# Performance work log

Measured on AMD Instinct MI355X. Metric: run time of the kernel, lower is better.

The kernel has to match this reference:

```python
import jax, jax.numpy as jnp
import numpy as np
from jax import lax

T, D_IN, D_OUT = 8192, 4096, 4096
N_ADAPT, RANK = 8, 16


def setup_inputs() -> dict:
    key = jax.random.key(0)
    ks = jax.random.split(key, 6)
    x = jax.random.normal(ks[0], (T, D_IN), jnp.float32)
    weight_indices = jax.random.randint(ks[1], (T,), 0, N_ADAPT, jnp.int64 if jax.config.jax_enable_x64 else jnp.int32)
    W_base = jax.random.normal(ks[2], (D_OUT, D_IN), jnp.float32) * 0.02
    A_buffer = jax.random.normal(ks[3], (N_ADAPT, D_IN, RANK), jnp.float32) * 0.02
    B_buffer = jax.random.normal(ks[4], (N_ADAPT, RANK, D_OUT), jnp.float32) * 0.02
    DeltaW = jax.random.normal(ks[5], (N_ADAPT, D_IN, D_OUT), jnp.float32) * 0.02
    return {"x": x, "weight_indices": weight_indices, "W_base": W_base,
            "A_buffer": A_buffer, "B_buffer": B_buffer, "DeltaW": DeltaW}


def _ldmm(indices, x, A, B, D):
    """Per-token adapter matmul: out[t] = x[t] @ (DeltaW[j] + A[j] @ B[j]), j = indices[t].
    Grouped by adapter via masked GEMMs (fixed small adapter count), jit-friendly."""
    n_adapt = A.shape[0]
    acc0 = jnp.zeros((x.shape[0], D.shape[2]), x.dtype)

    def body(acc, inp):
        a_id, A_a, B_a, D_a = inp
        mask = (indices == a_id)[:, None]
        xm = jnp.where(mask, x, jnp.zeros((), x.dtype))  # [T, in]
        W_eff = D_a + A_a @ B_a                          # [in, out]
        return acc + xm @ W_eff, None

    acc, _ = lax.scan(body, acc0, (jnp.arange(n_adapt), A, B, D))
    return acc


def reference(x, weight_indices, W_base, A_buffer, B_buffer, DeltaW):
    base = x @ W_base.T                                   # ColumnParallelLinear
    delta = _ldmm(weight_indices, x, A_buffer, B_buffer, DeltaW)
    # NOTE: source has `base_output = +output` (unary plus, likely a typo for `+=`);
    # we implement the intended fused semantics base + ldmm.
    return base + delta
```

## Files before the change

### kernel.cpp

```cpp
#include <hip/hip_runtime.h>


#define T_TOKENS 8192
#define DIM 4096
#define NADAPT 8
#define RANK 16

#define BM2 256
#define MAXT2 40
#define GRIDX2 (MAXT2 * 16)

#define BM1 128
#define MAXT1 72

typedef __attribute__((ext_vector_type(8))) short bf16x8;
typedef __attribute__((ext_vector_type(4))) float f32x4;

__device__ __forceinline__ unsigned short f2bf(float f) {
  union { float f; unsigned u; } v; v.f = f;
  unsigned r = v.u + 0x7FFFu + ((v.u >> 16) & 1u);
  return (unsigned short)(r >> 16);
}

__device__ __forceinline__ void gload_lds16(const void* g, void* l) {
  __builtin_amdgcn_global_load_lds(
      (const __attribute__((address_space(1))) void*)g,
      (__attribute__((address_space(3))) void*)l, 16, 0, 0);
}

template <int N> __device__ __forceinline__ void vmwait() {
  if constexpr (N == 0)      asm volatile("s_waitcnt vmcnt(0)" ::: "memory");
  else if constexpr (N == 4) asm volatile("s_waitcnt vmcnt(4)" ::: "memory");
  else if constexpr (N == 8) asm volatile("s_waitcnt vmcnt(8)" ::: "memory");
}

__global__ void prep_kernel(const int* __restrict__ idx, int* __restrict__ perm,
                            int* __restrict__ meta, int padm) {
  __shared__ int s_cnt[NADAPT];
  __shared__ int s_padoff[NADAPT + 1];
  __shared__ int s_wsum[16];
  const int tid = threadIdx.x;
  const int lane = tid & 63;
  const int wave = tid >> 6;

  if (tid < NADAPT) s_cnt[tid] = 0;
  __syncthreads();
  for (int t = tid; t < T_TOKENS; t += 1024) atomicAdd(&s_cnt[idx[t]], 1);
  __syncthreads();

  if (tid == 0) {
    int off = 0, nt = 0;
    for (int j = 0; j < NADAPT; ++j) {
      meta[j] = s_cnt[j];
      s_padoff[j] = off;
      const int c = s_cnt[j];
      const int ntj = (c + padm - 1) / padm;
      for (int i = 0; i < ntj; ++i) {
        meta[32 + 3 * nt + 0] = j;
        meta[32 + 3 * nt + 1] = off + i * padm;
        meta[32 + 3 * nt + 2] = min(padm, c - i * padm);
        ++nt;
      }
      off += ntj * padm;
    }
    s_padoff[NADAPT] = off;
    meta[17] = nt;
    for (int j = 0; j <= NADAPT; ++j) meta[8 + j] = s_padoff[j];
  }
  __syncthreads();

  const int total_pad = s_padoff[NADAPT];
  for (int t = tid; t < total_pad; t += 1024) perm[t] = -1;
  __syncthreads();

  for (int j = 0; j < NADAPT; ++j) {
    int base = s_padoff[j];
    for (int c0 = 0; c0 < T_TOKENS; c0 += 1024) {
      const int t = c0 + tid;
      const int flag = (idx[t] == j) ? 1 : 0;
      const unsigned long long bal = __ballot(flag);
      const int wpos = __popcll(bal & ((1ULL << lane) - 1ULL));
      if (lane == 0) s_wsum[wave] = __popcll(bal);
      __syncthreads();
      int woff = 0, ctot = 0;
      for (int w = 0; w < 16; ++w) {
        const int v = s_wsum[w];
        if (w < wave) woff += v;
        ctot += v;
      }
      if (flag) perm[base + woff + wpos] = t;
      base += ctot;
      __syncthreads();
    }
  }
}

__global__ void convert_x_kernel(const float* __restrict__ x,
                                 unsigned short* __restrict__ xb) {
  const long long i = (long long)blockIdx.x * 256 + threadIdx.x;
  const float4* x4 = (const float4*)x;
  const float4 a = x4[2 * i];
  const float4 b = x4[2 * i + 1];
  uint4 o;
  o.x = (unsigned)f2bf(a.x) | ((unsigned)f2bf(a.y) << 16);
  o.y = (unsigned)f2bf(a.z) | ((unsigned)f2bf(a.w) << 16);
  o.z = (unsigned)f2bf(b.x) | ((unsigned)f2bf(b.y) << 16);
  o.w = (unsigned)f2bf(b.z) | ((unsigned)f2bf(b.w) << 16);
  ((uint4*)xb)[i] = o;
}

__global__ __launch_bounds__(256) void build_wtot_all_kernel(
    const float* __restrict__ Wb, const float* __restrict__ Am,
    const float* __restrict__ Bm, const float* __restrict__ DW,
    unsigned short* __restrict__ Wt) {
  const int i0 = blockIdx.x << 6;
  const int o0 = blockIdx.y << 6;
  __shared__ float Dl[2][64 * 64];
  __shared__ float Alt[2][16][68];
  __shared__ float Bl[2][16][68];
  const int tid = threadIdx.x;
  const int to = (tid >> 4) << 2;
  const int ti = (tid & 15) << 2;

  float4 wbr[4];
#pragma unroll
  for (int m = 0; m < 4; ++m)
    wbr[m] = *(const float4*)(Wb + (size_t)(o0 + to + m) * DIM + i0 + ti);

  const int di = tid >> 4;
  const int do4 = (tid & 15) << 2;
  const int ar_i = tid >> 2, ar_r4 = (tid & 3) << 2;
  const int br_r = tid >> 4, br_o4 = (tid & 15) << 2;

  float4 dwr[4], ar, brv;
  {
    const float* dwp = DW + (size_t)i0 * DIM + o0;
#pragma unroll
    for (int q = 0; q < 4; ++q)
      dwr[q] = *(const float4*)(dwp + (size_t)(q * 16 + di) * DIM + do4);
    ar = *(const float4*)(Am + ((size_t)(i0 + ar_i)) * RANK + ar_r4);
    brv = *(const float4*)(Bm + (size_t)br_r * DIM + o0 + br_o4);
  }
#pragma unroll
  for (int q = 0; q < 4; ++q) {
    const int i = q * 16 + di;
    const int iq = i >> 2, ie = i & 3;
#pragma unroll
    for (int k = 0; k < 4; ++k) {
      const int o = do4 + k;
      Dl[0][o * 64 + (((iq ^ (o & 15)) << 2) | ie)] = ((const float*)&dwr[q])[k];
    }
  }
#pragma unroll
  for (int k = 0; k < 4; ++k) Alt[0][ar_r4 + k][ar_i] = ((const float*)&ar)[k];
  *(float4*)&Bl[0][br_r][br_o4] = brv;
  __syncthreads();

  for (int j = 0; j < NADAPT; ++j) {
    const int pb = j & 1;
    if (j + 1 < NADAPT) {
      const float* dwp = DW + ((size_t)(j + 1) * DIM + i0) * DIM + o0;
#pragma unroll
      for (int q = 0; q < 4; ++q)
        dwr[q] = *(const float4*)(dwp + (size_t)(q * 16 + di) * DIM + do4);
      ar = *(const float4*)(Am + ((size_t)(j + 1) * DIM + i0 + ar_i) * RANK + ar_r4);
      brv = *(const float4*)(Bm + ((size_t)(j + 1) * RANK + br_r) * DIM + o0 + br_o4);
    }
    float acc[4][4];
#pragma unroll
    for (int m = 0; m < 4; ++m) {
      const int o = to + m;
      const float4 d = *(const float4*)&Dl[pb][o * 64 + (((ti >> 2) ^ (o & 15)) << 2)];
      acc[m][0] = wbr[m].x + d.x; acc[m][1] = wbr[m].y + d.y;
      acc[m][2] = wbr[m].z + d.z; acc[m][3] = wbr[m].w + d.w;
    }
#pragma unroll
    for (int r = 0; r < RANK; ++r) {
      const float4 av = *(const float4*)&Alt[pb][r][ti];
      const float4 bv = *(const float4*)&Bl[pb][r][to];
#pragma unroll
      for (int m = 0; m < 4; ++m) {
        const float b = ((const float*)&bv)[m];
        acc[m][0] += b * av.x; acc[m][1] += b * av.y;
        acc[m][2] += b * av.z; acc[m][3] += b * av.w;
      }
    }
#pragma unroll
    for (int m = 0; m < 4; ++m) {
      const int o = to + m;
      const unsigned lo = (unsigned)f2bf(acc[m][0]) | ((unsigned)f2bf(acc[m][1]) << 16);
      const unsigned hi = (unsigned)f2bf(acc[m][2]) | ((unsigned)f2bf(acc[m][3]) << 16);
      uint2 pk; pk.x = lo; pk.y = hi;
      *(uint2*)(Wt + ((size_t)j * DIM + o0 + o) * DIM + i0 + ti) = pk;
    }
    if (j + 1 < NADAPT) {
      const int nb = pb ^ 1;
#pragma unroll
      for (int q = 0; q < 4; ++q) {
        const int i = q * 16 + di;
        const int iq = i >> 2, ie = i & 3;
#pragma unroll
        for (int k = 0; k < 4; ++k) {
          const int o = do4 + k;
          Dl[nb][o * 64 + (((iq ^ (o & 15)) << 2) | ie)] = ((const float*)&dwr[q])[k];
        }
      }
#pragma unroll
      for (int k = 0; k < 4; ++k) Alt[nb][ar_r4 + k][ar_i] = ((const float*)&ar)[k];
      *(float4*)&Bl[nb][br_r][br_o4] = brv;
      __syncthreads();
    }
  }
}

__global__ __launch_bounds__(256) void build_wtot_kernel(
    const float* __restrict__ Wb, const float* __restrict__ Am,
    const float* __restrict__ Bm, const float* __restrict__ DW,
    unsigned short* __restrict__ Wt, int j0) {
  const int jj = blockIdx.z;
  const int j = j0 + jj;
  const int i0 = blockIdx.x << 6;
  const int o0 = blockIdx.y << 6;
  __shared__ float Dl[64 * 64];
  __shared__ float Alt[16][68];
  __shared__ float Bl[16][68];
  const int tid = threadIdx.x;

  const float* dwp = DW + ((size_t)j * DIM + i0) * DIM + o0;
#pragma unroll
  for (int q = 0; q < 4; ++q) {
    const int lin = q * 256 + tid;
    const int i = lin >> 4;
    const int o4 = (lin & 15) << 2;
    const float4 v = *(const float4*)(dwp + (size_t)i * DIM + o4);
    const int iq = i >> 2, ie = i & 3;
#pragma unroll
    for (int k = 0; k < 4; ++k) {
      const int o = o4 + k;
      Dl[o * 64 + (((iq ^ (o & 15)) << 2) | ie)] = ((const float*)&v)[k];
    }
  }
  {
    const int ai = tid >> 2, r4 = (tid & 3) << 2;
    const float4 v = *(const float4*)(Am + ((size_t)j * DIM + i0 + ai) * RANK + r4);
#pragma unroll
    for (int k = 0; k < 4; ++k) Alt[r4 + k][ai] = ((const float*)&v)[k];
  }
  {
    const int br = tid >> 4, bo4 = (tid & 15) << 2;
    const float4 v = *(const float4*)(Bm + ((size_t)j * RANK + br) * DIM + o0 + bo4);
    *(float4*)&Bl[br][bo4] = v;
  }
  __syncthreads();

  const int to = (tid >> 4) << 2;
  const int ti = (tid & 15) << 2;
  float acc[4][4];

#pragma unroll
  for (int m = 0; m < 4; ++m) {
    const int o = to + m;
    const float4 w = *(const float4*)(Wb + (size_t)(o0 + o) * DIM + i0 + ti);
    const float4 d = *(const float4*)&Dl[o * 64 + (((ti >> 2) ^ (o & 15)) << 2)];
    acc[m][0] = w.x + d.x; acc[m][1] = w.y + d.y;
    acc[m][2] = w.z + d.z; acc[m][3] = w.w + d.w;
  }
#pragma unroll
  for (int r = 0; r < RANK; ++r) {
    const float4 av = *(const float4*)&Alt[r][ti];
    const float4 bv = *(const float4*)&Bl[r][to];
#pragma unroll
    for (int m = 0; m < 4; ++m) {
      const float b = ((const float*)&bv)[m];
      acc[m][0] += b * av.x; acc[m][1] += b * av.y;
      acc[m][2] += b * av.z; acc[m][3] += b * av.w;
    }
  }
#pragma unroll
  for (int m = 0; m < 4; ++m) {
    const int o = to + m;
    const unsigned lo = (unsigned)f2bf(acc[m][0]) | ((unsigned)f2bf(acc[m][1]) << 16);
    const unsigned hi = (unsigned)f2bf(acc[m][2]) | ((unsigned)f2bf(acc[m][3]) << 16);
    uint2 pk; pk.x = lo; pk.y = hi;
    *(uint2*)(Wt + ((size_t)jj * DIM + o0 + o) * DIM + i0 + ti) = pk;
  }
}

template <int BUF, int KK, int MQ, int VME, int SGRP, int SOP, int SKH, bool DOST>
__device__ __forceinline__ void do_phase(
    char* smem, int tid, int stile,
    const unsigned short* const* aB, const unsigned short* const* bB,
    const int* aoff, const int* boff, bf16x8* bfr, f32x4 (*acc)[4]) {
  const int grp = (BUF * 2 + KK) * 16384;
  if constexpr (MQ == 0) {
#pragma unroll
    for (int n = 0; n < 4; ++n)
      bfr[n] = *(const bf16x8*)(smem + 65536 + grp + boff[n]);
  }
  bf16x8 afr[4];
#pragma unroll
  for (int i = 0; i < 4; ++i)
    afr[i] = *(const bf16x8*)(smem + grp + aoff[MQ * 4 + i]);
  if constexpr (DOST) {
    const unsigned short* const* bs = SOP ? bB : aB;
#pragma unroll
    for (int q = 0; q < 2; ++q)
      gload_lds16(bs[q] + stile * 64 + SKH * 32,
                  smem + SOP * 65536 + SGRP * 16384 + q * 8192 + tid * 16);
  }
  __builtin_amdgcn_s_barrier();
  asm volatile("s_waitcnt lgkmcnt(0)" ::: "memory");
  __builtin_amdgcn_s_setprio(1);
#pragma unroll
  for (int i = 0; i < 4; ++i)
#pragma unroll
    for (int n = 0; n < 4; ++n)
      acc[MQ * 4 + i][n] =
          __builtin_amdgcn_mfma_f32_16x16x32_bf16(afr[i], bfr[n], acc[MQ * 4 + i][n], 0, 0, 0);
  __builtin_amdgcn_s_setprio(0);
  vmwait<VME>();
  __builtin_amdgcn_s_barrier();
}

template <int SGRP, int SOP, int SKH>
__device__ __forceinline__ void do_stage(
    char* smem, int tid, int stile,
    const unsigned short* const* aB, const unsigned short* const* bB) {
  const unsigned short* const* bs = SOP ? bB : aB;
#pragma unroll
  for (int q = 0; q < 2; ++q)
    gload_lds16(bs[q] + stile * 64 + SKH * 32,
                smem + SOP * 65536 + SGRP * 16384 + q * 8192 + tid * 16);
}

__global__ __launch_bounds__(512, 2) void gemm8_kernel(
    const unsigned short* __restrict__ xb, const unsigned short* __restrict__ Wt,
    const int* __restrict__ perm, const int* __restrict__ meta,
    float* __restrict__ out, int j0, int npp) {
  extern __shared__ char smem[];
  const int ntiles = meta[17];
  const int flat = blockIdx.x;
  const int swz = (flat & 7) * (GRIDX2 / 8) + (flat >> 3);
  const int mt = swz >> 4;
  const int nt = swz & 15;
  if (mt >= ntiles) return;
  const int adapter = meta[32 + 3 * mt];
  if (adapter < j0 || adapter >= j0 + npp) return;
  const int slot = adapter - j0;
  const int pbase = meta[32 + 3 * mt + 1];
  const int nbase = nt << 8;

  const int tid = threadIdx.x;
  const int lane = tid & 63;
  const int wave = tid >> 6;
  const int wr = wave >> 2, wc = wave & 3;
  const int fr = lane & 15, kg = lane >> 4;

  int aoff[8], boff[4];
#pragma unroll
  for (int m = 0; m < 8; ++m) {
    const int row = wr * 128 + m * 16 + fr;
    const int r = row >> 1, hf = row & 1;
    const int c = ((hf << 2) | kg) ^ (r & 7);
    aoff[m] = r * 128 + c * 16;
  }
#pragma unroll
  for (int n = 0; n < 4; ++n) {
    const int row = wc * 64 + n * 16 + fr;
    const int r = row >> 1, hf = row & 1;
    const int c = ((hf << 2) | kg) ^ (r & 7);
    boff[n] = r * 128 + c * 16;
  }

  const unsigned short* aB[2];
  const unsigned short* bB[2];
#pragma unroll
  for (int q = 0; q < 2; ++q) {
    const int L = q * 512 + tid;
    const int r = L >> 3, c = L & 7;
    const int s = c ^ (r & 7);
    const int grow = 2 * r + (s >> 2);
    const int gk = (s & 3) << 3;
    int pr = perm[pbase + grow];
    if (pr < 0) pr = 0;
    aB[q] = xb + (size_t)pr * DIM + gk;
    bB[q] = Wt + ((size_t)slot * DIM + nbase + grow) * DIM + gk;
  }

  const f32x4 zero = {0.f, 0.f, 0.f, 0.f};
  f32x4 acc[8][4];
#pragma unroll
  for (int m = 0; m < 8; ++m)
#pragma unroll
    for (int n = 0; n < 4; ++n) acc[m][n] = zero;
  bf16x8 bfr[4];

  do_stage<0, 0, 0>(smem, tid, 0, aB, bB);
  do_stage<0, 1, 0>(smem, tid, 0, aB, bB);
  do_stage<1, 0, 1>(smem, tid, 0, aB, bB);
  do_stage<1, 1, 1>(smem, tid, 0, aB, bB);
  do_stage<2, 0, 0>(smem, tid, 1, aB, bB);
  do_stage<2, 1, 0>(smem, tid, 1, aB, bB);
  vmwait<8>();
  __builtin_amdgcn_s_barrier();

  for (int it = 0; it < 31; ++it) {
    const int t1 = 2 * it + 1, t2 = 2 * it + 2, t3 = 2 * it + 3;
    do_phase<0, 0, 0, -1, 3, 0, 1, true>(smem, tid, t1, aB, bB, aoff, boff, bfr, acc);
    do_phase<0, 0, 1,  8, 3, 1, 1, true>(smem, tid, t1, aB, bB, aoff, boff, bfr, acc);
    do_phase<0, 1, 0, -1, 0, 0, 0, true>(smem, tid, t2, aB, bB, aoff, boff, bfr, acc);
    do_phase<0, 1, 1,  8, 0, 1, 0, true>(smem, tid, t2, aB, bB, aoff, boff, bfr, acc);
    do_phase<1, 0, 0, -1, 1, 0, 1, true>(smem, tid, t2, aB, bB, aoff, boff, bfr, acc);
    do_phase<1, 0, 1,  8, 1, 1, 1, true>(smem, tid, t2, aB, bB, aoff, boff, bfr, acc);
    do_phase<1, 1, 0, -1, 2, 0, 0, true>(smem, tid, t3, aB, bB, aoff, boff, bfr, acc);
    do_phase<1, 1, 1,  8, 2, 1, 0, true>(smem, tid, t3, aB, bB, aoff, boff, bfr, acc);
  }
  do_phase<0, 0, 0, -1, 3, 0, 1, true >(smem, tid, 63, aB, bB, aoff, boff, bfr, acc);
  do_phase<0, 0, 1,  8, 3, 1, 1, true >(smem, tid, 63, aB, bB, aoff, boff, bfr, acc);
  do_phase<0, 1, 0, -1, 0, 0, 0, false>(smem, tid, 0,  aB, bB, aoff, boff, bfr, acc);
  do_phase<0, 1, 1,  4, 0, 0, 0, false>(smem, tid, 0,  aB, bB, aoff, boff, bfr, acc);
  do_phase<1, 0, 0, -1, 0, 0, 0, false>(smem, tid, 0,  aB, bB, aoff, boff, bfr, acc);
  do_phase<1, 0, 1,  0, 0, 0, 0, false>(smem, tid, 0,  aB, bB, aoff, boff, bfr, acc);
  do_phase<1, 1, 0, -1, 0, 0, 0, false>(smem, tid, 0,  aB, bB, aoff, boff, bfr, acc);
  do_phase<1, 1, 1, -1, 0, 0, 0, false>(smem, tid, 0,  aB, bB, aoff, boff, bfr, acc);

#pragma unroll
  for (int m = 0; m < 8; ++m) {
#pragma unroll
    for (int t = 0; t < 4; ++t) {
      const int rt = wr * 128 + m * 16 + kg * 4 + t;
      const int pr = perm[pbase + rt];
      if (pr < 0) continue;
      float* orow = out + (size_t)pr * DIM + nbase + wc * 64;
#pragma unroll
      for (int n = 0; n < 4; ++n) orow[n * 16 + fr] = acc[m][n][t];
    }
  }
}

template <bool USE_XB>
__global__ __launch_bounds__(256) void gemm_kernel(
    const unsigned short* __restrict__ xb, const float* __restrict__ xf,
    const unsigned short* __restrict__ Wt,
    const int* __restrict__ perm, const int* __restrict__ meta,
    float* __restrict__ out, int j0, int npp) {
  const int ntiles = meta[17];
  const int mt = blockIdx.x;
  if (mt >= ntiles) return;
  const int adapter = meta[32 + 3 * mt];
  if (adapter < j0 || adapter >= j0 + npp) return;
  const int slot = adapter - j0;
  const int nt = blockIdx.y;
  const int pbase = meta[32 + 3 * mt + 1];
  const int nbase = nt << 7;

  __shared__ __align__(16) unsigned short As[BM1 * 64];
  __shared__ __align__(16) unsigned short Bs[BM1 * 64];

  const int tid = threadIdx.x;
  const int lane = tid & 63;
  const int wave = tid >> 6;

  const unsigned short* aSrcB[4];
  const float* aSrcF[4];
  const unsigned short* bSrc[4];
  unsigned short* aDst[4];
  unsigned short* bDst[4];
#pragma unroll
  for (int q = 0; q < 4; ++q) {
    const int c = wave * 4 + q;
    const int r = c * 8 + (lane >> 3);
    int pr = perm[pbase + r];
    if (pr < 0) pr = 0;
    if (USE_XB) aSrcB[q] = xb + (size_t)pr * DIM + (lane & 7) * 8;
    else        aSrcF[q] = xf + (size_t)pr * DIM + (lane & 7) * 8;
    bSrc[q] = Wt + ((size_t)slot * DIM + nbase + r) * DIM + (lane & 7) * 8;
    aDst[q] = As + c * 512;
    bDst[q] = Bs + c * 512;
  }

  const int wr = wave >> 1, wc = wave & 1;
  const int fr = lane & 15, kg = lane >> 4;

  const f32x4 zero = {0.f, 0.f, 0.f, 0.f};
  f32x4 acc[4][4];
#pragma unroll
  for (int m = 0; m < 4; ++m)
#pragma unroll
    for (int n = 0; n < 4; ++n) acc[m][n] = zero;

  for (int k0 = 0; k0 < DIM; k0 += 64) {
    if (USE_XB) {
#pragma unroll
      for (int q = 0; q < 4; ++q) gload_lds16(aSrcB[q] + k0, aDst[q]);
    } else {
#pragma unroll
      for (int q = 0; q < 4; ++q) {
        const float4 va = *(const float4*)(aSrcF[q] + k0);
        const float4 vb = *(const float4*)(aSrcF[q] + k0 + 4);
        union { bf16x8 v; unsigned short s[8]; } u;
        u.s[0] = f2bf(va.x); u.s[1] = f2bf(va.y); u.s[2] = f2bf(va.z); u.s[3] = f2bf(va.w);
        u.s[4] = f2bf(vb.x); u.s[5] = f2bf(vb.y); u.s[6] = f2bf(vb.z); u.s[7] = f2bf(vb.w);
        *(bf16x8*)(aDst[q] + lane * 8) = u.v;
      }
    }
#pragma unroll
    for (int q = 0; q < 4; ++q) gload_lds16(bSrc[q] + k0, bDst[q]);
    __syncthreads();
#pragma unroll
    for (int kk = 0; kk < 2; ++kk) {
      bf16x8 a[4], b[4];
#pragma unroll
      for (int m = 0; m < 4; ++m)
        a[m] = *(const bf16x8*)(&As[(wr * 64 + m * 16 + fr) * 64 + kk * 32 + kg * 8]);
#pragma unroll
      for (int n = 0; n < 4; ++n)
        b[n] = *(const bf16x8*)(&Bs[(wc * 64 + n * 16 + fr) * 64 + kk * 32 + kg * 8]);
#pragma unroll
      for (int m = 0; m < 4; ++m)
#pragma unroll
        for (int n = 0; n < 4; ++n)
          acc[m][n] = __builtin_amdgcn_mfma_f32_16x16x32_bf16(a[m], b[n], acc[m][n], 0, 0, 0);
    }
    __syncthreads();
  }

#pragma unroll
  for (int m = 0; m < 4; ++m) {
#pragma unroll
    for (int t = 0; t < 4; ++t) {
      const int rt = wr * 64 + m * 16 + kg * 4 + t;
      const int pr = perm[pbase + rt];
      if (pr < 0) continue;
      float* orow = out + (size_t)pr * DIM + nbase + wc * 64;
#pragma unroll
      for (int n = 0; n < 4; ++n) orow[n * 16 + fr] = acc[m][n][t];
    }
  }
}

extern "C" void kernel_launch(void* const* d_in, const int* in_sizes, int n_in,
                              void* d_out, int out_size, void* d_ws, size_t ws_size,
                              hipStream_t stream) {
  const float* x  = (const float*)d_in[0];
  const int* widx = (const int*)d_in[1];
  const float* Wb = (const float*)d_in[2];
  const float* Am = (const float*)d_in[3];
  const float* Bm = (const float*)d_in[4];
  const float* DW = (const float*)d_in[5];
  float* out = (float*)d_out;

  const size_t XB_BYTES = (size_t)T_TOKENS * DIM * 2;
  const size_t WT1_BYTES = (size_t)DIM * DIM * 2;
  const size_t PM_BYTES = 16384 * sizeof(int) + 4096;

  int npp = 0;
  bool use_xb = true;
  for (int cand = NADAPT; cand >= 1; cand >>= 1) {
    if (XB_BYTES + (size_t)cand * WT1_BYTES + PM_BYTES <= ws_size) { npp = cand; break; }
  }
  if (npp == 0) { npp = 1; use_xb = false; }

  bool use8 = use_xb &&
      (hipFuncSetAttribute((const void*)gemm8_kernel,
                           hipFuncAttributeMaxDynamicSharedMemorySize, 131072) == hipSuccess);

  char* ws = (char*)d_ws;
  unsigned short* xb = (unsigned short*)ws;
  unsigned short* Wt = (unsigned short*)(ws + (use_xb ? XB_BYTES : 0));
  char* tail = (char*)Wt + (size_t)npp * WT1_BYTES;
  int* perm = (int*)tail;
  int* meta = (int*)(tail + 16384 * sizeof(int));

  prep_kernel<<<dim3(1), dim3(1024), 0, stream>>>(widx, perm, meta, use8 ? BM2 : BM1);
  if (use_xb)
    convert_x_kernel<<<dim3(T_TOKENS * DIM / (256 * 8)), dim3(256), 0, stream>>>(x, xb);

  if (npp == NADAPT) {
    build_wtot_all_kernel<<<dim3(DIM / 64, DIM / 64), dim3(256), 0, stream>>>(
        Wb, Am, Bm, DW, Wt);
    if (use8)
      gemm8_kernel<<<dim3(GRIDX2), dim3(512), 131072, stream>>>(
          xb, Wt, perm, meta, out, 0, NADAPT);
    else
      gemm_kernel<true><<<dim3(MAXT1, DIM / 128), dim3(256), 0, stream>>>(
          xb, nullptr, Wt, perm, meta, out, 0, NADAPT);
  } else {
    const int passes = NADAPT / npp;
    for (int p = 0; p < passes; ++p) {
      const int j0 = p * npp;
      build_wtot_kernel<<<dim3(DIM / 64, DIM / 64, npp), dim3(256), 0, stream>>>(
          Wb, Am, Bm, DW, Wt, j0);
      if (use_xb)
        gemm_kernel<true><<<dim3(MAXT1, DIM / 128), dim3(256), 0, stream>>>(
            xb, nullptr, Wt, perm, meta, out, j0, npp);
      else
        gemm_kernel<false><<<dim3(MAXT1, DIM / 128), dim3(256), 0, stream>>>(
            nullptr, x, Wt, perm, meta, out, j0, npp);
    }
  }
}
```

Measured before the change: 642.7 us.

## Split tail M-tiles into a separate 128-row kernel to balance the grid

```diff
diff --git a/kernel.cpp b/kernel.cpp
--- a/kernel.cpp
+++ b/kernel.cpp
@@ -8,7 +8,7 @@
 
 #define BM2 256
 #define MAXT2 40
-#define GRIDX2 (MAXT2 * 16)
+#define GRIDX2 512
 
 #define BM1 128
 #define MAXT1 72
@@ -438,6 +438,91 @@
   }
 }
 
+__global__ __launch_bounds__(256) void gemm_tail_kernel(
+    const unsigned short* __restrict__ xb, const unsigned short* __restrict__ Wt,
+    const int* __restrict__ perm, const int* __restrict__ meta,
+    float* __restrict__ out) {
+  const int ntiles = meta[17];
+  const int mt = 32 + (blockIdx.x >> 1);
+  if (mt >= ntiles) return;
+  const int half = blockIdx.x & 1;
+  const int adapter = meta[32 + 3 * mt];
+  const int pbase = meta[32 + 3 * mt + 1] + half * 128;
+  if (half * 128 >= meta[32 + 3 * mt + 2]) return;
+  const int nt = blockIdx.y;
+  const int nbase = nt << 7;
+
+  __shared__ __align__(16) unsigned short As[BM1 * 64];
+  __shared__ __align__(16) unsigned short Bs[BM1 * 64];
+
+  const int tid = threadIdx.x;
+  const int lane = tid & 63;
+  const int wave = tid >> 6;
+
+  const unsigned short* aSrcB[4];
+  const unsigned short* bSrc[4];
+  unsigned short* aDst[4];
+  unsigned short* bDst[4];
+#pragma unroll
+  for (int q = 0; q < 4; ++q) {
+    const int c = wave * 4 + q;
+    const int r = c * 8 + (lane >> 3);
+    int pr = perm[pbase + r];
+    if (pr < 0) pr = 0;
+    aSrcB[q] = xb + (size_t)pr * DIM + (lane & 7) * 8;
+    bSrc[q] = Wt + ((size_t)adapter * DIM + nbase + r) * DIM + (lane & 7) * 8;
+    aDst[q] = As + c * 512;
+    bDst[q] = Bs + c * 512;
+  }
+
+  const int wr = wave >> 1, wc = wave & 1;
+  const int fr = lane & 15, kg = lane >> 4;
+
+  const f32x4 zero = {0.f, 0.f, 0.f, 0.f};
+  f32x4 acc[4][4];
+#pragma unroll
+  for (int m = 0; m < 4; ++m)
+#pragma unroll
+    for (int n = 0; n < 4; ++n) acc[m][n] = zero;
+
+  for (int k0 = 0; k0 < DIM; k0 += 64) {
+#pragma unroll
+    for (int q = 0; q < 4; ++q) gload_lds16(aSrcB[q] + k0, aDst[q]);
+#pragma unroll
+    for (int q = 0; q < 4; ++q) gload_lds16(bSrc[q] + k0, bDst[q]);
+    __syncthreads();
+#pragma unroll
+    for (int kk = 0; kk < 2; ++kk) {
+      bf16x8 a[4], b[4];
+#pragma unroll
+      for (int m = 0; m < 4; ++m)
+        a[m] = *(const bf16x8*)(&As[(wr * 64 + m * 16 + fr) * 64 + kk * 32 + kg * 8]);
+#pragma unroll
+      for (int n = 0; n < 4; ++n)
+        b[n] = *(const bf16x8*)(&Bs[(wc * 64 + n * 16 + fr) * 64 + kk * 32 + kg * 8]);
+#pragma unroll
+      for (int m = 0; m < 4; ++m)
+#pragma unroll
+        for (int n = 0; n < 4; ++n)
+          acc[m][n] = __builtin_amdgcn_mfma_f32_16x16x32_bf16(a[m], b[n], acc[m][n], 0, 0, 0);
+    }
+    __syncthreads();
+  }
+
+#pragma unroll
+  for (int m = 0; m < 4; ++m) {
+#pragma unroll
+    for (int t = 0; t < 4; ++t) {
+      const int rt = wr * 64 + m * 16 + kg * 4 + t;
+      const int pr = perm[pbase + rt];
+      if (pr < 0) continue;
+      float* orow = out + (size_t)pr * DIM + nbase + wc * 64;
+#pragma unroll
+      for (int n = 0; n < 4; ++n) orow[n * 16 + fr] = acc[m][n][t];
+    }
+  }
+}
+
 template <bool USE_XB>
 __global__ __launch_bounds__(256) void gemm_kernel(
     const unsigned short* __restrict__ xb, const float* __restrict__ xf,
@@ -579,12 +664,15 @@
   if (npp == NADAPT) {
     build_wtot_all_kernel<<<dim3(DIM / 64, DIM / 64), dim3(256), 0, stream>>>(
         Wb, Am, Bm, DW, Wt);
-    if (use8)
+    if (use8) {
       gemm8_kernel<<<dim3(GRIDX2), dim3(512), 131072, stream>>>(
           xb, Wt, perm, meta, out, 0, NADAPT);
-    else
+      gemm_tail_kernel<<<dim3(16, DIM / 128), dim3(256), 0, stream>>>(
+          xb, Wt, perm, meta, out);
+    } else {
       gemm_kernel<true><<<dim3(MAXT1, DIM / 128), dim3(256), 0, stream>>>(
           xb, nullptr, Wt, perm, meta, out, 0, NADAPT);
+    }
   } else {
     const int passes = NADAPT / npp;
     for (int p = 0; p < passes; ++p) {
```

Result: no change. 632.8 us (-1.5%).

## Split tail M-tiles of grouped GEMM with split-K and atomic accumulation

Applied to the files above, without the earlier changes.

```diff
diff --git a/kernel.cpp b/kernel.cpp
--- a/kernel.cpp
+++ b/kernel.cpp
@@ -7,8 +7,7 @@
 #define RANK 16
 
 #define BM2 256
-#define MAXT2 40
-#define GRIDX2 (MAXT2 * 16)
+#define GRIDX2 512
 
 #define BM1 128
 #define MAXT1 72
@@ -95,6 +94,24 @@
   }
 }
 
+__global__ __launch_bounds__(256) void zero_tail_kernel(
+    const int* __restrict__ perm, const int* __restrict__ meta,
+    float* __restrict__ out) {
+  const int ntiles = meta[17];
+  const int mt = 32 + (int)(blockIdx.x >> 1);
+  if (mt >= ntiles) return;
+  const int half = blockIdx.x & 1;
+  const int pbase = meta[32 + 3 * mt + 1] + half * 128;
+  const int row = threadIdx.x >> 1;
+  const int c0 = blockIdx.y * 128 + (threadIdx.x & 1) * 64;
+  const int pr = perm[pbase + row];
+  if (pr < 0) return;
+  float4* p = (float4*)(out + (size_t)pr * DIM + c0);
+  const float4 z = {0.f, 0.f, 0.f, 0.f};
+#pragma unroll
+  for (int k = 0; k < 16; ++k) p[k] = z;
+}
+
 __global__ void convert_x_kernel(const float* __restrict__ x,
                                  unsigned short* __restrict__ xb) {
   const long long i = (long long)blockIdx.x * 256 + threadIdx.x;
@@ -333,22 +350,31 @@
                 smem + SOP * 65536 + SGRP * 16384 + q * 8192 + tid * 16);
 }
 
+template <int NTILES, bool TAILK>
 __global__ __launch_bounds__(512, 2) void gemm8_kernel(
     const unsigned short* __restrict__ xb, const unsigned short* __restrict__ Wt,
     const int* __restrict__ perm, const int* __restrict__ meta,
-    float* __restrict__ out, int j0, int npp) {
+    float* __restrict__ out) {
   extern __shared__ char smem[];
   const int ntiles = meta[17];
   const int flat = blockIdx.x;
-  const int swz = (flat & 7) * (GRIDX2 / 8) + (flat >> 3);
-  const int mt = swz >> 4;
-  const int nt = swz & 15;
+  int mt, nt, kc;
+  if (TAILK) {
+    kc = flat >> 7;
+    const int r = flat & 127;
+    mt = 32 + (r >> 4);
+    nt = r & 15;
+  } else {
+    const int swz = (flat & 7) * (GRIDX2 / 8) + (flat >> 3);
+    mt = swz >> 4;
+    nt = swz & 15;
+    kc = 0;
+  }
   if (mt >= ntiles) return;
   const int adapter = meta[32 + 3 * mt];
-  if (adapter < j0 || adapter >= j0 + npp) return;
-  const int slot = adapter - j0;
   const int pbase = meta[32 + 3 * mt + 1];
   const int nbase = nt << 8;
+  const size_t kbase = (size_t)kc * (NTILES * 64);
 
   const int tid = threadIdx.x;
   const int lane = tid & 63;
@@ -383,8 +409,8 @@
     const int gk = (s & 3) << 3;
     int pr = perm[pbase + grow];
     if (pr < 0) pr = 0;
-    aB[q] = xb + (size_t)pr * DIM + gk;
-    bB[q] = Wt + ((size_t)slot * DIM + nbase + grow) * DIM + gk;
+    aB[q] = xb + (size_t)pr * DIM + gk + kbase;
+    bB[q] = Wt + ((size_t)adapter * DIM + nbase + grow) * DIM + gk + kbase;
   }
 
   const f32x4 zero = {0.f, 0.f, 0.f, 0.f};
@@ -404,7 +430,7 @@
   vmwait<8>();
   __builtin_amdgcn_s_barrier();
 
-  for (int it = 0; it < 31; ++it) {
+  for (int it = 0; it < NTILES / 2 - 1; ++it) {
     const int t1 = 2 * it + 1, t2 = 2 * it + 2, t3 = 2 * it + 3;
     do_phase<0, 0, 0, -1, 3, 0, 1, true>(smem, tid, t1, aB, bB, aoff, boff, bfr, acc);
     do_phase<0, 0, 1,  8, 3, 1, 1, true>(smem, tid, t1, aB, bB, aoff, boff, bfr, acc);
@@ -415,14 +441,14 @@
     do_phase<1, 1, 0, -1, 2, 0, 0, true>(smem, tid, t3, aB, bB, aoff, boff, bfr, acc);
     do_phase<1, 1, 1,  8, 2, 1, 0, true>(smem, tid, t3, aB, bB, aoff, boff, bfr, acc);
   }
-  do_phase<0, 0, 0, -1, 3, 0, 1, true >(smem, tid, 63, aB, bB, aoff, boff, bfr, acc);
-  do_phase<0, 0, 1,  8, 3, 1, 1, true >(smem, tid, 63, aB, bB, aoff, boff, bfr, acc);
-  do_phase<0, 1, 0, -1, 0, 0, 0, false>(smem, tid, 0,  aB, bB, aoff, boff, bfr, acc);
-  do_phase<0, 1, 1,  4, 0, 0, 0, false>(smem, tid, 0,  aB, bB, aoff, boff, bfr, acc);
-  do_phase<1, 0, 0, -1, 0, 0, 0, false>(smem, tid, 0,  aB, bB, aoff, boff, bfr, acc);
-  do_phase<1, 0, 1,  0, 0, 0, 0, false>(smem, tid, 0,  aB, bB, aoff, boff, bfr, acc);
-  do_phase<1, 1, 0, -1, 0, 0, 0, false>(smem, tid, 0,  aB, bB, aoff, boff, bfr, acc);
-  do_phase<1, 1, 1, -1, 0, 0, 0, false>(smem, tid, 0,  aB, bB, aoff, boff, bfr, acc);
+  do_phase<0, 0, 0, -1, 3, 0, 1, true >(smem, tid, NTILES - 1, aB, bB, aoff, boff, bfr, acc);
+  do_phase<0, 0, 1,  8, 3, 1, 1, true >(smem, tid, NTILES - 1, aB, bB, aoff, boff, bfr, acc);
+  do_phase<0, 1, 0, -1, 0, 0, 0, false>(smem, tid, 0, aB, bB, aoff, boff, bfr, acc);
+  do_phase<0, 1, 1,  4, 0, 0, 0, false>(smem, tid, 0, aB, bB, aoff, boff, bfr, acc);
+  do_phase<1, 0, 0, -1, 0, 0, 0, false>(smem, tid, 0, aB, bB, aoff, boff, bfr, acc);
+  do_phase<1, 0, 1,  0, 0, 0, 0, false>(smem, tid, 0, aB, bB, aoff, boff, bfr, acc);
+  do_phase<1, 1, 0, -1, 0, 0, 0, false>(smem, tid, 0, aB, bB, aoff, boff, bfr, acc);
+  do_phase<1, 1, 1, -1, 0, 0, 0, false>(smem, tid, 0, aB, bB, aoff, boff, bfr, acc);
 
 #pragma unroll
   for (int m = 0; m < 8; ++m) {
@@ -433,7 +459,10 @@
       if (pr < 0) continue;
       float* orow = out + (size_t)pr * DIM + nbase + wc * 64;
 #pragma unroll
-      for (int n = 0; n < 4; ++n) orow[n * 16 + fr] = acc[m][n][t];
+      for (int n = 0; n < 4; ++n) {
+        if (TAILK) atomicAdd(&orow[n * 16 + fr], acc[m][n][t]);
+        else       orow[n * 16 + fr] = acc[m][n][t];
+      }
     }
   }
 }
@@ -561,8 +590,10 @@
   }
   if (npp == 0) { npp = 1; use_xb = false; }
 
-  bool use8 = use_xb &&
-      (hipFuncSetAttribute((const void*)gemm8_kernel,
+  bool use8 = (npp == NADAPT) &&
+      (hipFuncSetAttribute((const void*)gemm8_kernel<64, false>,
+                           hipFuncAttributeMaxDynamicSharedMemorySize, 131072) == hipSuccess) &&
+      (hipFuncSetAttribute((const void*)gemm8_kernel<16, true>,
                            hipFuncAttributeMaxDynamicSharedMemorySize, 131072) == hipSuccess);
 
   char* ws = (char*)d_ws;
@@ -577,14 +608,19 @@
     convert_x_kernel<<<dim3(T_TOKENS * DIM / (256 * 8)), dim3(256), 0, stream>>>(x, xb);
 
   if (npp == NADAPT) {
+    if (use8)
+      zero_tail_kernel<<<dim3(16, DIM / 128), dim3(256), 0, stream>>>(perm, meta, out);
     build_wtot_all_kernel<<<dim3(DIM / 64, DIM / 64), dim3(256), 0, stream>>>(
         Wb, Am, Bm, DW, Wt);
-    if (use8)
-      gemm8_kernel<<<dim3(GRIDX2), dim3(512), 131072, stream>>>(
-          xb, Wt, perm, meta, out, 0, NADAPT);
-    else
+    if (use8) {
+      gemm8_kernel<64, false><<<dim3(GRIDX2), dim3(512), 131072, stream>>>(
+          xb, Wt, perm, meta, out);
+      gemm8_kernel<16, true><<<dim3(512), dim3(512), 131072, stream>>>(
+          xb, Wt, perm, meta, out);
+    } else {
       gemm_kernel<true><<<dim3(MAXT1, DIM / 128), dim3(256), 0, stream>>>(
           xb, nullptr, Wt, perm, meta, out, 0, NADAPT);
+    }
   } else {
     const int passes = NADAPT / npp;
     for (int p = 0; p < passes; ++p) {
```

Result: faster. 629.0 us (-2.1%).
